# Performance work log

Hardware: AMD Instinct MI355X
Metric: run time of the kernel (lower is better)

Reference implementation:

```python
import jax, jax.numpy as jnp
import numpy as np

B, L, V = 8192, 64, 28
LATENT = 32
PAD_TOKEN, EOS_TOKEN = 26, 27
EPS = 1e-7
LETTER_FREQS = jnp.array([0.0817, 0.0149, 0.0278, 0.0425, 0.127, 0.0223, 0.0202,
                          0.0609, 0.0697, 0.0015, 0.0077, 0.0403, 0.0241, 0.0675,
                          0.0751, 0.0193, 0.001, 0.0599, 0.0633, 0.0906, 0.0276,
                          0.0098, 0.0236, 0.0015, 0.0197, 0.0007], dtype=jnp.float32)
FREQS_PAD = jnp.pad(LETTER_FREQS, (0, V - 26))  # tf.pad to VOCAB_SIZE


def setup_inputs() -> dict:
    key = jax.random.key(0)
    k1, k2, k3, k4, k5 = jax.random.split(key, 5)
    x = jax.random.normal(k1, (B, L, V), dtype=jnp.float32)
    # decoder output is a softmax -> valid probability tensor
    reconstruction = jax.nn.softmax(jax.random.normal(k2, (B, L, V), dtype=jnp.float32), axis=-1)
    z_mean = jax.random.normal(k3, (B, LATENT), dtype=jnp.float32)
    z_log_var = jax.random.normal(k4, (B, LATENT), dtype=jnp.float32)
    classifier_score = jax.random.uniform(k5, (B, 1), dtype=jnp.float32)
    return {"x": x, "reconstruction": reconstruction, "z_mean": z_mean,
            "z_log_var": z_log_var, "classifier_score": classifier_score}


def _total_loss(x, reconstruction, z_mean, z_log_var, classifier_score):
    targets = jnp.argmax(x, axis=-1)                       # [B, L] int
    mask = (targets != PAD_TOKEN).astype(jnp.float32)      # [B, L]

    # sparse categorical CE on probabilities (tf clips probs)
    p_tgt = jnp.take_along_axis(reconstruction, targets[..., None], axis=-1)[..., 0]
    per_position_loss = -jnp.log(jnp.clip(p_tgt, EPS, 1.0))
    reconstruction_loss = jnp.sum(per_position_loss * mask) / jnp.sum(mask)

    kl_loss = -0.5 * jnp.mean(1.0 + z_log_var - jnp.square(z_mean) - jnp.exp(z_log_var))

    classifier_loss = -jnp.mean(jnp.log(classifier_score + EPS))

    # consecutive similarity: sum_i i^2.5 * sum_j prod(adjacent[:, j:j+i])
    mask_adj = (targets[:, 1:] != PAD_TOKEN).astype(jnp.float32)       # [B, L-1]
    adjacent = jnp.sum(reconstruction[:, 1:] * reconstruction[:, :-1], axis=-1) * mask_adj
    Lm1 = L - 1
    pos = jnp.arange(Lm1)

    def step(carry, k):
        # k = i - 1; p[:, j] holds prod(adjacent[:, j:j+k]) from previous step
        p, acc = carry
        valid = (pos < (Lm1 - k)).astype(adjacent.dtype)               # [L-1]
        shifted = jnp.roll(adjacent, -k, axis=1) * valid               # adjacent[:, j+k], 0 past end
        p = p * shifted                                                # window length k+1; invalid j -> 0
        w = jnp.power((k + 1).astype(jnp.float32), 2.5)
        acc = acc + w * jnp.sum(p)
        return (p, acc), None

    init = (adjacent, jnp.sum(adjacent))                               # i = 1, weight 1^2.5
    (_, consecutive_similarity), _ = jax.lax.scan(step, init, jnp.arange(1, Lm1))

    mask_exp = jnp.logical_and(targets != PAD_TOKEN, targets != EOS_TOKEN).astype(jnp.float32)[:, :, None]
    mean_letter_probs = jnp.sum(reconstruction * mask_exp, axis=(0, 1)) / jnp.sum(mask_exp)
    frequency_penalty = jnp.sum(jnp.maximum(0.0, mean_letter_probs - FREQS_PAD))

    total_loss = (reconstruction_loss + 0.1 * kl_loss + 2.0 * classifier_loss
                  + 0.2 * consecutive_similarity + 0.5 * frequency_penalty)
    return total_loss


def reference(x, reconstruction, z_mean, z_log_var, classifier_score):
    return _total_loss(x, reconstruction, z_mean, z_log_var, classifier_score)
```

## Files before the change

kernel.cpp:

```cpp
#include <hip/hip_runtime.h>
#include <math.h>

#define VB 28
#define LL 64
#define PAD_TOK 26
#define EOS_TOK 27
#define NSLOT 34
#define REPL 16
#define RPW 4
#define RSTRIDE 29

constexpr double csqrt_(double x) {
  double g = x > 1.0 ? x : 1.0;
  for (int i = 0; i < 60; ++i) g = 0.5 * (g + x / g);
  return g;
}
struct WTab { float w[64]; };
constexpr WTab make_wtab() {
  WTab t{};
  for (int k = 0; k < 64; ++k) {
    double n = (double)(k + 1);
    t.w[k] = (float)(n * n * csqrt_(n));
  }
  return t;
}
constexpr WTab WTAB = make_wtab();

__device__ __forceinline__ float wave_red(float v) {
  #pragma unroll
  for (int o = 32; o > 0; o >>= 1) v += __shfl_down(v, o, 64);
  return v;
}

__global__ __launch_bounds__(256, 2) void vae_main(
    const float* __restrict__ x, const float* __restrict__ rec,
    const float* __restrict__ zm, const float* __restrict__ zlv,
    const float* __restrict__ cs, float* __restrict__ ws,
    int nrows, int nz, int nc, int nblocks) {
  __shared__ float row_s[4][65 * RSTRIDE];
  __shared__ float adj_s[4][128];
  __shared__ float red[4][NSLOT];
  __shared__ int   tgt_s[4][64];
  const int lane = threadIdx.x & 63;
  const int wid  = threadIdx.x >> 6;
  adj_s[wid][64 + lane] = 0.f;
  __builtin_amdgcn_wave_barrier();

  float loss_acc = 0.f, mask_cnt = 0.f, mexp_cnt = 0.f;
  float consec0 = 0.f, consec1 = 0.f;
  float vocab[VB];
  #pragma unroll
  for (int v = 0; v < VB; ++v) vocab[v] = 0.f;

  const int wave_id = blockIdx.x * 4 + wid;
  const int row0 = wave_id * RPW;

  float4 xb[2][7], rb[2][7];
  #pragma unroll
  for (int q = 0; q < 2; ++q) {
    const int row = row0 + q;
    if (row < nrows) {
      const size_t base = ((size_t)row * LL + lane) * VB;
      const float4* xp = reinterpret_cast<const float4*>(x + base);
      const float4* rp = reinterpret_cast<const float4*>(rec + base);
      #pragma unroll
      for (int i = 0; i < 7; ++i) { xb[q][i] = xp[i]; rb[q][i] = rp[i]; }
    }
  }

  #pragma unroll
  for (int it = 0; it < RPW; ++it) {
    const int row = row0 + it;
    if (row >= nrows) break;
    const int cur = it & 1;

    float best = -INFINITY, pt = 0.f;
    int tgt = 0;
    #pragma unroll
    for (int i = 0; i < 7; ++i) {
      const float4 xq = xb[cur][i];
      const float4 rq = rb[cur][i];
      row_s[wid][lane * RSTRIDE + i*4 + 0] = rq.x;
      row_s[wid][lane * RSTRIDE + i*4 + 1] = rq.y;
      row_s[wid][lane * RSTRIDE + i*4 + 2] = rq.z;
      row_s[wid][lane * RSTRIDE + i*4 + 3] = rq.w;
      if (xq.x > best) { best = xq.x; tgt = i*4+0; pt = rq.x; }
      if (xq.y > best) { best = xq.y; tgt = i*4+1; pt = rq.y; }
      if (xq.z > best) { best = xq.z; tgt = i*4+2; pt = rq.z; }
      if (xq.w > best) { best = xq.w; tgt = i*4+3; pt = rq.w; }
    }
    tgt_s[wid][lane] = tgt;
    __builtin_amdgcn_wave_barrier();

    if (it + 2 < RPW && row + 2 < nrows) {
      const size_t base = ((size_t)(row + 2) * LL + lane) * VB;
      const float4* xp = reinterpret_cast<const float4*>(x + base);
      const float4* rp = reinterpret_cast<const float4*>(rec + base);
      #pragma unroll
      for (int i = 0; i < 7; ++i) { xb[cur][i] = xp[i]; rb[cur][i] = rp[i]; }
    }

    const float mask = (tgt != PAD_TOK) ? 1.f : 0.f;
    const float mexp = (tgt != PAD_TOK && tgt != EOS_TOK) ? 1.f : 0.f;
    loss_acc += -__logf(fminf(fmaxf(pt, 1e-7f), 1.f)) * mask;
    mask_cnt += mask;
    mexp_cnt += mexp;

    const float* own = &row_s[wid][lane * RSTRIDE];
    const float* nbr = own + RSTRIDE;
    float adj = 0.f;
    #pragma unroll
    for (int v = 0; v < VB; ++v) {
      const float ov = own[v];
      vocab[v] += ov * mexp;
      adj += ov * nbr[v];
    }
    const int tgtn = (lane < 63) ? tgt_s[wid][lane + 1] : PAD_TOK;
    adj = (lane < 63 && tgtn != PAD_TOK) ? adj : 0.f;

    __builtin_amdgcn_wave_barrier();
    adj_s[wid][lane] = adj;
    __builtin_amdgcn_wave_barrier();

    const float* ap = &adj_s[wid][lane];
    float p = adj;
    consec0 += p;
    #pragma unroll
    for (int k = 1; k <= 62; k += 2) {
      p *= ap[k];
      consec1 += WTAB.w[k] * p;
      if (k + 1 <= 62) {
        p *= ap[k + 1];
        consec0 += WTAB.w[k + 1] * p;
      }
    }
    __builtin_amdgcn_wave_barrier();
  }
  float consec_acc = consec0 + consec1;

  const int gid = blockIdx.x * 256 + threadIdx.x;
  const int gstride = nblocks * 256;
  float kl = 0.f, cl = 0.f;
  for (int i = gid; i < nz; i += gstride) {
    const float m = zm[i], lv = zlv[i];
    kl += 1.f + lv - m * m - __expf(lv);
  }
  for (int i = gid; i < nc; i += gstride) cl += __logf(cs[i] + 1e-7f);

  loss_acc   = wave_red(loss_acc);
  mask_cnt   = wave_red(mask_cnt);
  consec_acc = wave_red(consec_acc);
  mexp_cnt   = wave_red(mexp_cnt);
  kl         = wave_red(kl);
  cl         = wave_red(cl);

  float* tw = &row_s[wid][0];
  __builtin_amdgcn_wave_barrier();
  #pragma unroll
  for (int v = 0; v < VB; ++v) tw[lane * RSTRIDE + v] = vocab[v];
  __builtin_amdgcn_wave_barrier();
  float vs = 0.f;
  if (lane < VB) {
    float s0 = 0.f, s1 = 0.f, s2 = 0.f, s3 = 0.f;
    #pragma unroll
    for (int pidx = 0; pidx < 64; pidx += 4) {
      s0 += tw[(pidx + 0) * RSTRIDE + lane];
      s1 += tw[(pidx + 1) * RSTRIDE + lane];
      s2 += tw[(pidx + 2) * RSTRIDE + lane];
      s3 += tw[(pidx + 3) * RSTRIDE + lane];
    }
    vs = (s0 + s1) + (s2 + s3);
  }
  __builtin_amdgcn_wave_barrier();

  if (lane == 0) {
    red[wid][0] = loss_acc; red[wid][1] = mask_cnt;
    red[wid][2] = consec_acc; red[wid][3] = mexp_cnt;
    red[wid][4] = kl; red[wid][5] = cl;
  }
  if (lane < VB) red[wid][6 + lane] = vs;
  __syncthreads();
  if (threadIdx.x < NSLOT) {
    const int t = threadIdx.x;
    const int b = blockIdx.x & (REPL - 1);
    atomicAdd(&ws[t * (REPL * 32) + b * 32],
              red[0][t] + red[1][t] + red[2][t] + red[3][t]);
  }
}

__global__ void vae_finalize(const float* __restrict__ ws, float* __restrict__ out,
                             float nz, float nc) {
  if (threadIdx.x == 0 && blockIdx.x == 0) {
    const float freqs[VB] = {0.0817f,0.0149f,0.0278f,0.0425f,0.127f,0.0223f,
      0.0202f,0.0609f,0.0697f,0.0015f,0.0077f,0.0403f,0.0241f,0.0675f,0.0751f,
      0.0193f,0.001f,0.0599f,0.0633f,0.0906f,0.0276f,0.0098f,0.0236f,0.0015f,
      0.0197f,0.0007f,0.f,0.f};
    float fin[NSLOT];
    #pragma unroll
    for (int t = 0; t < NSLOT; ++t) {
      float s = 0.f;
      #pragma unroll
      for (int b = 0; b < REPL; ++b) s += ws[t * (REPL * 32) + b * 32];
      fin[t] = s;
    }
    const float rec_loss = fin[0] / fin[1];
    const float kl_loss  = -0.5f * fin[4] / nz;
    const float cls_loss = -fin[5] / nc;
    const float inv_mexp = 1.f / fin[3];
    float fp = 0.f;
    #pragma unroll
    for (int v = 0; v < VB; ++v)
      fp += fmaxf(0.f, fin[6 + v] * inv_mexp - freqs[v]);
    out[0] = rec_loss + 0.1f * kl_loss + 2.f * cls_loss
           + 0.2f * fin[2] + 0.5f * fp;
  }
}

extern "C" void kernel_launch(void* const* d_in, const int* in_sizes, int n_in,
                              void* d_out, int out_size, void* d_ws, size_t ws_size,
                              hipStream_t stream) {
  const float* x   = (const float*)d_in[0];
  const float* rec = (const float*)d_in[1];
  const float* zm  = (const float*)d_in[2];
  const float* zlv = (const float*)d_in[3];
  const float* cs  = (const float*)d_in[4];
  float* out = (float*)d_out;
  float* ws  = (float*)d_ws;

  const int nrows = in_sizes[0] / (LL * VB);
  const int nz    = in_sizes[2];
  const int nc    = in_sizes[4];

  int nblocks = (nrows + 4 * RPW - 1) / (4 * RPW);
  if (nblocks < 1) nblocks = 1;

  hipMemsetAsync(d_ws, 0, NSLOT * REPL * 32 * sizeof(float), stream);
  vae_main<<<nblocks, 256, 0, stream>>>(x, rec, zm, zlv, cs, ws,
                                        nrows, nz, nc, nblocks);
  vae_finalize<<<1, 64, 0, stream>>>(ws, out, (float)nz, (float)nc);
}
```

Measured before the change: 161.4 us.

## Coalesce row loads across lanes and redistribute via shared-memory argmax partials

Global loads now have each lane read consecutive float4s, so a wave's accesses are contiguous, instead of each lane reading its own 112-byte position. The partial argmax over each float4 is done in registers, and the per-position argmax is finished by reading 7 partials from shared memory. Prefetch drops from two rows to one, which frees registers, and the occupancy hint of 2 is removed. The neighbour target now comes from a wave shuffle instead of shared memory. In exchange there is more shared-memory traffic and less latency hiding from the shallower prefetch.

```diff
diff --git a/kernel.cpp b/kernel.cpp
--- a/kernel.cpp
+++ b/kernel.cpp
@@ -8,7 +8,7 @@
 #define NSLOT 34
 #define REPL 16
 #define RPW 4
-#define RSTRIDE 29
+#define RS 29
 
 constexpr double csqrt_(double x) {
   double g = x > 1.0 ? x : 1.0;
@@ -32,18 +32,20 @@
   return v;
 }
 
-__global__ __launch_bounds__(256, 2) void vae_main(
+__global__ __launch_bounds__(256) void vae_main(
     const float* __restrict__ x, const float* __restrict__ rec,
     const float* __restrict__ zm, const float* __restrict__ zlv,
     const float* __restrict__ cs, float* __restrict__ ws,
     int nrows, int nz, int nc, int nblocks) {
-  __shared__ float row_s[4][65 * RSTRIDE];
+  __shared__ float rec_s[4][65 * RS];
+  __shared__ float maxv_s[4][448];
+  __shared__ int   maxi_s[4][448];
   __shared__ float adj_s[4][128];
   __shared__ float red[4][NSLOT];
-  __shared__ int   tgt_s[4][64];
   const int lane = threadIdx.x & 63;
   const int wid  = threadIdx.x >> 6;
   adj_s[wid][64 + lane] = 0.f;
+  if (lane < RS) rec_s[wid][64 * RS + lane] = 0.f;
   __builtin_amdgcn_wave_barrier();
 
   float loss_acc = 0.f, mask_cnt = 0.f, mexp_cnt = 0.f;
@@ -55,59 +57,60 @@
   const int wave_id = blockIdx.x * 4 + wid;
   const int row0 = wave_id * RPW;
 
-  float4 xb[2][7], rb[2][7];
-  #pragma unroll
-  for (int q = 0; q < 2; ++q) {
-    const int row = row0 + q;
-    if (row < nrows) {
-      const size_t base = ((size_t)row * LL + lane) * VB;
-      const float4* xp = reinterpret_cast<const float4*>(x + base);
-      const float4* rp = reinterpret_cast<const float4*>(rec + base);
-      #pragma unroll
-      for (int i = 0; i < 7; ++i) { xb[q][i] = xp[i]; rb[q][i] = rp[i]; }
-    }
+  float4 xb[7], rb[7];
+  if (row0 < nrows) {
+    const float4* xp = reinterpret_cast<const float4*>(x) + (size_t)row0 * 448;
+    const float4* rp = reinterpret_cast<const float4*>(rec) + (size_t)row0 * 448;
+    #pragma unroll
+    for (int i = 0; i < 7; ++i) { xb[i] = xp[i*64 + lane]; rb[i] = rp[i*64 + lane]; }
   }
 
   #pragma unroll
   for (int it = 0; it < RPW; ++it) {
     const int row = row0 + it;
     if (row >= nrows) break;
-    const int cur = it & 1;
-
-    float best = -INFINITY, pt = 0.f;
-    int tgt = 0;
+
     #pragma unroll
     for (int i = 0; i < 7; ++i) {
-      const float4 xq = xb[cur][i];
-      const float4 rq = rb[cur][i];
-      row_s[wid][lane * RSTRIDE + i*4 + 0] = rq.x;
-      row_s[wid][lane * RSTRIDE + i*4 + 1] = rq.y;
-      row_s[wid][lane * RSTRIDE + i*4 + 2] = rq.z;
-      row_s[wid][lane * RSTRIDE + i*4 + 3] = rq.w;
-      if (xq.x > best) { best = xq.x; tgt = i*4+0; pt = rq.x; }
-      if (xq.y > best) { best = xq.y; tgt = i*4+1; pt = rq.y; }
-      if (xq.z > best) { best = xq.z; tgt = i*4+2; pt = rq.z; }
-      if (xq.w > best) { best = xq.w; tgt = i*4+3; pt = rq.w; }
-    }
-    tgt_s[wid][lane] = tgt;
-    __builtin_amdgcn_wave_barrier();
-
-    if (it + 2 < RPW && row + 2 < nrows) {
-      const size_t base = ((size_t)(row + 2) * LL + lane) * VB;
-      const float4* xp = reinterpret_cast<const float4*>(x + base);
-      const float4* rp = reinterpret_cast<const float4*>(rec + base);
+      const int u = i * 64 + lane;
+      const int p = u / 7;
+      const int m = u - p * 7;
+      float* dst = &rec_s[wid][p * RS + 4 * m];
+      const float4 rq = rb[i];
+      dst[0] = rq.x; dst[1] = rq.y; dst[2] = rq.z; dst[3] = rq.w;
+      const float4 xq = xb[i];
+      float mx = xq.x; int mi = 0;
+      if (xq.y > mx) { mx = xq.y; mi = 1; }
+      if (xq.z > mx) { mx = xq.z; mi = 2; }
+      if (xq.w > mx) { mx = xq.w; mi = 3; }
+      maxv_s[wid][u] = mx;
+      maxi_s[wid][u] = 4 * m + mi;
+    }
+    __builtin_amdgcn_wave_barrier();
+
+    if (it + 1 < RPW && row + 1 < nrows) {
+      const float4* xp = reinterpret_cast<const float4*>(x) + (size_t)(row + 1) * 448;
+      const float4* rp = reinterpret_cast<const float4*>(rec) + (size_t)(row + 1) * 448;
       #pragma unroll
-      for (int i = 0; i < 7; ++i) { xb[cur][i] = xp[i]; rb[cur][i] = rp[i]; }
-    }
-
+      for (int i = 0; i < 7; ++i) { xb[i] = xp[i*64 + lane]; rb[i] = rp[i*64 + lane]; }
+    }
+
+    float best = -INFINITY; int tgt = 0;
+    #pragma unroll
+    for (int m = 0; m < 7; ++m) {
+      const float v = maxv_s[wid][7 * lane + m];
+      const int  ix = maxi_s[wid][7 * lane + m];
+      if (v > best) { best = v; tgt = ix; }
+    }
+    const float pt = rec_s[wid][lane * RS + tgt];
     const float mask = (tgt != PAD_TOK) ? 1.f : 0.f;
     const float mexp = (tgt != PAD_TOK && tgt != EOS_TOK) ? 1.f : 0.f;
     loss_acc += -__logf(fminf(fmaxf(pt, 1e-7f), 1.f)) * mask;
     mask_cnt += mask;
     mexp_cnt += mexp;
 
-    const float* own = &row_s[wid][lane * RSTRIDE];
-    const float* nbr = own + RSTRIDE;
+    const float* own = &rec_s[wid][lane * RS];
+    const float* nbr = own + RS;
     float adj = 0.f;
     #pragma unroll
     for (int v = 0; v < VB; ++v) {
@@ -115,7 +118,7 @@
       vocab[v] += ov * mexp;
       adj += ov * nbr[v];
     }
-    const int tgtn = (lane < 63) ? tgt_s[wid][lane + 1] : PAD_TOK;
+    const int tgtn = __shfl_down(tgt, 1, 64);
     adj = (lane < 63 && tgtn != PAD_TOK) ? adj : 0.f;
 
     __builtin_amdgcn_wave_barrier();
@@ -154,20 +157,20 @@
   kl         = wave_red(kl);
   cl         = wave_red(cl);
 
-  float* tw = &row_s[wid][0];
-  __builtin_amdgcn_wave_barrier();
-  #pragma unroll
-  for (int v = 0; v < VB; ++v) tw[lane * RSTRIDE + v] = vocab[v];
+  float* tw = &rec_s[wid][0];
+  __builtin_amdgcn_wave_barrier();
+  #pragma unroll
+  for (int v = 0; v < VB; ++v) tw[lane * RS + v] = vocab[v];
   __builtin_amdgcn_wave_barrier();
   float vs = 0.f;
   if (lane < VB) {
     float s0 = 0.f, s1 = 0.f, s2 = 0.f, s3 = 0.f;
     #pragma unroll
     for (int pidx = 0; pidx < 64; pidx += 4) {
-      s0 += tw[(pidx + 0) * RSTRIDE + lane];
-      s1 += tw[(pidx + 1) * RSTRIDE + lane];
-      s2 += tw[(pidx + 2) * RSTRIDE + lane];
-      s3 += tw[(pidx + 3) * RSTRIDE + lane];
+      s0 += tw[(pidx + 0) * RS + lane];
+      s1 += tw[(pidx + 1) * RS + lane];
+      s2 += tw[(pidx + 2) * RS + lane];
+      s3 += tw[(pidx + 3) * RS + lane];
     }
     vs = (s0 + s1) + (s2 + s3);
   }
```

Result: no change. 163.9 us (+1.6%).
